# Kernel tuning notes

Hardware: AMD Instinct MI355X
Metric: run time of the kernel (lower is better)

## Reference

```python
import jax, jax.numpy as jnp
import numpy as np

N, K, GS = 11008, 4096, 128   # outfeatures, infeatures, group_size
INTER, KSTRIDE = 4, 64        # interleave, kstride from pack_intweight
B, S = 4, 2048
NG = K // GS                  # number of quantization groups


def _pack_np(q):
    """Replicates torch pack_intweight on an (N, K) int array of 4-bit values."""
    P = q.reshape(N, K // 32, 32)
    P = P.reshape(N, K // 32, 4, 4, 2).transpose(0, 1, 3, 2, 4).reshape(N, K // 32, 32)
    P = P.reshape(N, K // 32, 4, 8).reshape(N, K // 32, 4, 4, 2)
    P = P.transpose(0, 1, 2, 4, 3).reshape(N, K)
    P = P.reshape(N // INTER, INTER, K // KSTRIDE, KSTRIDE).transpose(0, 2, 1, 3)
    P = P.reshape(N // INTER, K // KSTRIDE, KSTRIDE, INTER)
    P = P[..., 0] | (P[..., 1] << 4) | (P[..., 2] << 8) | (P[..., 3] << 12)
    # uint16 bit pattern stored in int32 (schema has no int16)
    return P.reshape(N // INTER, K).astype(np.int32)


def setup_inputs() -> dict:
    rng = np.random.default_rng(0)
    q_unpacked = rng.integers(0, 16, size=(N, K), dtype=np.int64)  # int4 codes
    qweight = jnp.asarray(_pack_np(q_unpacked))

    key = jax.random.key(0)
    k1, k2, k3, k4 = jax.random.split(key, 4)
    x = jax.random.normal(k1, (B, S, K), dtype=jnp.float16)
    scales = (jax.random.uniform(k2, (NG, N), dtype=jnp.float32) * 0.01 + 0.005).astype(jnp.float16)
    scaled_zeros = (jax.random.normal(k3, (NG, N), dtype=jnp.float32) * 0.05).astype(jnp.float16)
    bias = (jax.random.normal(k4, (N,), dtype=jnp.float32) * 0.02).astype(jnp.float16)
    return {"x": x, "qweight": qweight, "scales": scales,
            "scaled_zeros": scaled_zeros, "bias": bias}


def _unpack(qweight):
    """Inverse of pack_intweight: (N//4, K) packed -> (N, K) int4 codes."""
    # split the 4 nibbles packed per 16-bit word
    nib = jnp.stack([(qweight >> (4 * i)) & 0xF for i in range(4)], axis=-1)  # (N//4, K, 4)
    # invert the interleave/kstride step
    t = nib.reshape(N // INTER, K // KSTRIDE, INTER, KSTRIDE)
    t = t.transpose(0, 2, 1, 3).reshape(N, K)
    # invert the second 32-lane shuffle
    t = t.reshape(N, K // 32, 4, 2, 4).transpose(0, 1, 2, 4, 3).reshape(N, K // 32, 32)
    # invert the first 32-lane shuffle
    t = t.reshape(N, K // 32, 4, 4, 2).transpose(0, 1, 3, 2, 4).reshape(N, K)
    return t


def reference(x, qweight, scales, scaled_zeros, bias):
    q = _unpack(qweight).astype(jnp.float16)                      # (N, K) codes 0..15
    s = scales.T[:, :, None]                                      # (N, NG, 1)
    z = scaled_zeros.T[:, :, None]                                # (N, NG, 1); stored as -zero*scale
    # w = q * scale + scaled_zeros  (== (q - zero) * scale)
    W = (q.reshape(N, NG, GS) * s + z).reshape(N, K)              # fp16 dequant
    return jnp.einsum('bsk,nk->bsn', x, W) + bias                 # (B, S, N)
```

## Files before the change

### kernel.cpp

```cpp
#include <hip/hip_runtime.h>
#include <hip/hip_bf16.h>

#define K_TOT 4096
#define N_TOT 11008
#define LDP 72

typedef __bf16 bf16x8 __attribute__((ext_vector_type(8)));
typedef float  f32x4  __attribute__((ext_vector_type(4)));
typedef float  f32x8  __attribute__((ext_vector_type(8)));

typedef __attribute__((address_space(1))) unsigned gu32;
typedef __attribute__((address_space(3))) unsigned lu32;

__device__ __forceinline__ void gload_lds16(const void* g, void* l) {
    __builtin_amdgcn_global_load_lds((gu32*)g, (lu32*)l, 16, 0, 0);
}

__global__ __launch_bounds__(256)
void dequant_w(const int* __restrict__ Qw, const float* __restrict__ Sc,
               const float* __restrict__ Zr, __bf16* __restrict__ Wb)
{
    const int t   = blockIdx.x * 256 + threadIdx.x;
    const int c8  = t & (K_TOT / 8 - 1);
    const int r4  = t >> 9;
    const int kp0 = c8 * 8;
    const int n   = r4 * 4 + ((kp0 >> 4) & 3);
    const int kq  = kp0 >> 6;
    const int hf  = (kp0 >> 3) & 1;
    const int kb  = kq * 64 + hf * 32;

    const int4 wa = *(const int4*)(Qw + (size_t)r4 * K_TOT + kp0);
    const int4 wb = *(const int4*)(Qw + (size_t)r4 * K_TOT + kp0 + 4);
    const int g = kb >> 7;
    const float s = Sc[(size_t)g * N_TOT + n];
    const float z = Zr[(size_t)g * N_TOT + n];

    const int w8[8] = {wa.x, wa.y, wa.z, wa.w, wb.x, wb.y, wb.z, wb.w};
    bf16x8 ov[4];
    #pragma unroll
    for (int uu = 0; uu < 8; ++uu) {
        const unsigned v = (unsigned)w8[uu] & 0xFFFFu;
        #pragma unroll
        for (int i = 0; i < 4; ++i)
            ov[i][uu] = (__bf16)fmaf((float)((v >> (4 * i)) & 0xFu), s, z);
    }
    __bf16* o = Wb + (size_t)n * K_TOT + kb;
    #pragma unroll
    for (int i = 0; i < 4; ++i) *(bf16x8*)(o + i * 8) = ov[i];
}

__global__ __launch_bounds__(256)
void convert_x(const float* __restrict__ X, __bf16* __restrict__ Xb, long total8)
{
    const long t = (long)blockIdx.x * 256 + threadIdx.x;
    if (t >= total8) return;
    f32x8 v = *(const f32x8*)(X + t * 8);
    bf16x8 o;
    #pragma unroll
    for (int j = 0; j < 8; ++j) o[j] = (__bf16)v[j];
    *(bf16x8*)(Xb + t * 8) = o;
}

__global__ __launch_bounds__(512, 2)
void gemm256(const __bf16* __restrict__ A, const __bf16* __restrict__ B,
             const float* __restrict__ Bias, float* __restrict__ C, int gridM)
{
    extern __shared__ char lds_raw[];

    const int tid  = threadIdx.x;
    const int lane = tid & 63;
    const int wid  = tid >> 6;
    const int l15  = lane & 15;
    const int lhi  = lane >> 4;

    const int nwg = gridDim.x;
    int wg = blockIdx.x;
    if ((nwg & 7) == 0) wg = (wg & 7) * (nwg >> 3) + (wg >> 3);
    const int bx  = wg % gridM;
    const int by  = wg / gridM;
    const int bm0 = bx * 256;
    const int bn0 = by * 256;

    const int wm = (wid >> 2) * 128;
    const int wn = (wid & 3) * 64;

    const int sr   = lane >> 3;
    const int scol = ((lane & 7) ^ sr) * 8;

    const __bf16* ap[4]; const __bf16* bp[4];
    #pragma unroll
    for (int j = 0; j < 4; ++j) {
        const int c = wid * 4 + j;
        ap[j] = A + (size_t)(bm0 + c * 8 + sr) * K_TOT + scol;
        bp[j] = B + (size_t)(bn0 + c * 8 + sr) * K_TOT + scol;
    }

    char* buf0 = lds_raw;
    char* buf1 = lds_raw + 65536;
    const int ldsoff = wid * 4096;

    const unsigned rswz = (unsigned)((l15 & 7) << 4);

    f32x4 acc[8][4] = {};

    #pragma unroll
    for (int j = 0; j < 4; ++j) {
        gload_lds16(ap[j], buf0 + ldsoff + j * 1024);
        gload_lds16(bp[j], buf0 + 32768 + ldsoff + j * 1024);
    }

    char* cur = buf0; char* nxt = buf1;
    const int NT = K_TOT / 64;
    for (int t = 0; t < NT; ++t) {
        if (t + 1 < NT) {
            const int k1 = (t + 1) * 64;
            #pragma unroll
            for (int j = 0; j < 4; ++j) {
                gload_lds16(ap[j] + k1, nxt + ldsoff + j * 1024);
                gload_lds16(bp[j] + k1, nxt + 32768 + ldsoff + j * 1024);
            }
            asm volatile("s_waitcnt vmcnt(8)" ::: "memory");
        } else {
            asm volatile("s_waitcnt vmcnt(0)" ::: "memory");
        }
        __builtin_amdgcn_s_barrier();
        __builtin_amdgcn_sched_barrier(0);

        #pragma unroll
        for (int ks = 0; ks < 2; ++ks) {
            bf16x8 af[8], bfv[4];
            const unsigned cb = ((unsigned)(ks * 64 + lhi * 16)) ^ rswz;
            #pragma unroll
            for (int mi = 0; mi < 8; ++mi)
                af[mi] = *(const bf16x8*)(cur + (wm + mi * 16 + l15) * 128 + cb);
            #pragma unroll
            for (int ni = 0; ni < 4; ++ni)
                bfv[ni] = *(const bf16x8*)(cur + 32768 + (wn + ni * 16 + l15) * 128 + cb);
            __builtin_amdgcn_s_setprio(1);
            #pragma unroll
            for (int mi = 0; mi < 8; ++mi)
                #pragma unroll
                for (int ni = 0; ni < 4; ++ni)
                    acc[mi][ni] = __builtin_amdgcn_mfma_f32_16x16x32_bf16(
                        af[mi], bfv[ni], acc[mi][ni], 0, 0, 0);
            __builtin_amdgcn_s_setprio(0);
        }
        asm volatile("" ::: "memory");
        __builtin_amdgcn_s_barrier();
        __builtin_amdgcn_sched_barrier(0);
        char* tmp = cur; cur = nxt; nxt = tmp;
    }

    #pragma unroll
    for (int ni = 0; ni < 4; ++ni) {
        const int col = bn0 + wn + ni * 16 + l15;
        const float bv = Bias[col];
        #pragma unroll
        for (int mi = 0; mi < 8; ++mi) {
            const int row = bm0 + wm + mi * 16 + lhi * 4;
            #pragma unroll
            for (int r = 0; r < 4; ++r)
                C[(size_t)(row + r) * N_TOT + col] = acc[mi][ni][r] + bv;
        }
    }
}

__global__ __launch_bounds__(256)
void qgemm_fused(const float* __restrict__ X, const int* __restrict__ Qw,
                 const float* __restrict__ Sc, const float* __restrict__ Zr,
                 const float* __restrict__ Bias, float* __restrict__ C)
{
    __shared__ __bf16 As[128][LDP];
    __shared__ __bf16 Bs[128][LDP];

    const int tid  = threadIdx.x;
    const int lane = tid & 63;
    const int wid  = tid >> 6;
    const int l15  = lane & 15;
    const int lhi  = lane >> 4;

    const int bm0 = blockIdx.x * 128;
    const int bn0 = blockIdx.y * 128;
    const int wm  = (wid >> 1) * 64;
    const int wn  = (wid & 1) * 64;

    const int ar = tid >> 3;
    const int ac = (tid & 7) * 8;

    const int nl   = tid >> 1;
    const int half = tid & 1;
    const int n_g  = bn0 + nl;
    const int* qptr = Qw + (size_t)(n_g >> 2) * K_TOT + (nl & 3) * 16 + half * 8;
    const float* scp = Sc + n_g;
    const float* zrp = Zr + n_g;

    f32x4 acc[4][4] = {};

    for (int kt = 0; kt < K_TOT / 64; ++kt) {
        const int k0 = kt * 64;
        const int4 wa = *(const int4*)(qptr + k0);
        const int4 wb = *(const int4*)(qptr + k0 + 4);
        const float s = scp[(size_t)(kt >> 1) * N_TOT];
        const float z = zrp[(size_t)(kt >> 1) * N_TOT];

        f32x8 av[4];
        #pragma unroll
        for (int p = 0; p < 4; ++p)
            av[p] = *(const f32x8*)(X + (size_t)(bm0 + p * 32 + ar) * K_TOT + k0 + ac);

        const int w8[8] = {wa.x, wa.y, wa.z, wa.w, wb.x, wb.y, wb.z, wb.w};
        bf16x8 ov[4];
        #pragma unroll
        for (int uu = 0; uu < 8; ++uu) {
            const unsigned v = (unsigned)w8[uu] & 0xFFFFu;
            #pragma unroll
            for (int i = 0; i < 4; ++i)
                ov[i][uu] = (__bf16)fmaf((float)((v >> (4 * i)) & 0xFu), s, z);
        }
        #pragma unroll
        for (int p = 0; p < 4; ++p) {
            bf16x8 ab;
            #pragma unroll
            for (int j = 0; j < 8; ++j) ab[j] = (__bf16)av[p][j];
            *(bf16x8*)&As[p * 32 + ar][ac] = ab;
        }
        #pragma unroll
        for (int cc = 0; cc < 4; ++cc)
            *(bf16x8*)&Bs[nl][half * 32 + cc * 8] = ov[cc];

        __syncthreads();

        #pragma unroll
        for (int ks = 0; ks < 2; ++ks) {
            bf16x8 af[4], bfr[4];
            const int kc = ks * 32 + lhi * 8;
            #pragma unroll
            for (int mi = 0; mi < 4; ++mi)
                af[mi] = *(const bf16x8*)&As[wm + mi * 16 + l15][kc];
            #pragma unroll
            for (int ni = 0; ni < 4; ++ni)
                bfr[ni] = *(const bf16x8*)&Bs[wn + ni * 16 + l15][kc];
            #pragma unroll
            for (int mi = 0; mi < 4; ++mi)
                #pragma unroll
                for (int ni = 0; ni < 4; ++ni)
                    acc[mi][ni] = __builtin_amdgcn_mfma_f32_16x16x32_bf16(
                        af[mi], bfr[ni], acc[mi][ni], 0, 0, 0);
        }
        __syncthreads();
    }

    #pragma unroll
    for (int ni = 0; ni < 4; ++ni) {
        const int col = bn0 + wn + ni * 16 + l15;
        const float bv = Bias[col];
        #pragma unroll
        for (int mi = 0; mi < 4; ++mi) {
            const int row = bm0 + wm + mi * 16 + lhi * 4;
            #pragma unroll
            for (int r = 0; r < 4; ++r)
                C[(size_t)(row + r) * N_TOT + col] = acc[mi][ni][r] + bv;
        }
    }
}

extern "C" void kernel_launch(void* const* d_in, const int* in_sizes, int n_in,
                              void* d_out, int out_size, void* d_ws, size_t ws_size,
                              hipStream_t stream) {
    const float* X    = (const float*)d_in[0];
    const int*   Qw   = (const int*)d_in[1];
    const float* Sc   = (const float*)d_in[2];
    const float* Zr   = (const float*)d_in[3];
    const float* Bias = (const float*)d_in[4];
    float* C = (float*)d_out;

    const int M = in_sizes[0] / K_TOT;
    const size_t xb_bytes = (size_t)M * K_TOT * 2;
    const size_t wb_bytes = (size_t)N_TOT * K_TOT * 2;
    const size_t need = xb_bytes + wb_bytes;

    const int gridM = M / 256;
    const int nwg   = gridM * (N_TOT / 256);

    if (ws_size >= need && (M & 255) == 0 && (nwg & 7) == 0) {
        __bf16* Xb = (__bf16*)d_ws;
        __bf16* Wb = (__bf16*)((char*)d_ws + xb_bytes);

        const int nW = (N_TOT / 4) * (K_TOT / 8);
        dequant_w<<<nW / 256, 256, 0, stream>>>(Qw, Sc, Zr, Wb);

        const long total8 = (long)M * K_TOT / 8;
        convert_x<<<(int)((total8 + 255) / 256), 256, 0, stream>>>(X, Xb, total8);

        (void)hipFuncSetAttribute((const void*)gemm256,
                                  hipFuncAttributeMaxDynamicSharedMemorySize, 131072);
        gemm256<<<dim3(nwg), dim3(512), 131072, stream>>>(Xb, Wb, Bias, C, gridM);
    } else {
        dim3 grid(M / 128, N_TOT / 128);
        qgemm_fused<<<grid, dim3(256), 0, stream>>>(X, Qw, Sc, Zr, Bias, C);
    }
}
```

Baseline: 925.8 us.

## Switch GEMM to 256x128 tiles with a three-stage LDS pipeline

```diff
diff --git a/kernel.cpp b/kernel.cpp
--- a/kernel.cpp
+++ b/kernel.cpp
@@ -61,9 +61,14 @@
     *(bf16x8*)(Xb + t * 8) = o;
 }
 
-__global__ __launch_bounds__(512, 2)
-void gemm256(const __bf16* __restrict__ A, const __bf16* __restrict__ B,
-             const float* __restrict__ Bias, float* __restrict__ C, int gridM)
+#define STAGE_A(kt, r, dst) \
+    gload_lds16(apg + (size_t)(r) * 64 * K_TOT + (size_t)(kt) * 64, (dst) + wid * 1024 + (r) * 8192)
+#define STAGE_B(kt, r, dst) \
+    gload_lds16(bpg + (size_t)(r) * 64 * K_TOT + (size_t)(kt) * 64, (dst) + 32768 + wid * 1024 + (r) * 8192)
+
+__global__ __launch_bounds__(512, 1)
+void gemm256x128(const __bf16* __restrict__ A, const __bf16* __restrict__ B,
+                 const float* __restrict__ Bias, float* __restrict__ C, int gridM)
 {
     extern __shared__ char lds_raw[];
 
@@ -75,80 +80,93 @@
 
     const int nwg = gridDim.x;
     int wg = blockIdx.x;
-    if ((nwg & 7) == 0) wg = (wg & 7) * (nwg >> 3) + (wg >> 3);
+    wg = (wg & 7) * (nwg >> 3) + (wg >> 3);
     const int bx  = wg % gridM;
     const int by  = wg / gridM;
     const int bm0 = bx * 256;
-    const int bn0 = by * 256;
-
-    const int wm = (wid >> 2) * 128;
-    const int wn = (wid & 3) * 64;
+    const int bn0 = by * 128;
+
+    const int wm = (wid >> 1) * 64;
+    const int wn = (wid & 1) * 64;
 
     const int sr   = lane >> 3;
     const int scol = ((lane & 7) ^ sr) * 8;
-
-    const __bf16* ap[4]; const __bf16* bp[4];
-    #pragma unroll
-    for (int j = 0; j < 4; ++j) {
-        const int c = wid * 4 + j;
-        ap[j] = A + (size_t)(bm0 + c * 8 + sr) * K_TOT + scol;
-        bp[j] = B + (size_t)(bn0 + c * 8 + sr) * K_TOT + scol;
-    }
-
-    char* buf0 = lds_raw;
-    char* buf1 = lds_raw + 65536;
-    const int ldsoff = wid * 4096;
+    const __bf16* apg = A + (size_t)(bm0 + wid * 8 + sr) * K_TOT + scol;
+    const __bf16* bpg = B + (size_t)(bn0 + wid * 8 + sr) * K_TOT + scol;
+
+    char* s0 = lds_raw;
+    char* s1 = lds_raw + 49152;
+    char* s2 = lds_raw + 98304;
 
     const unsigned rswz = (unsigned)((l15 & 7) << 4);
 
-    f32x4 acc[8][4] = {};
-
-    #pragma unroll
-    for (int j = 0; j < 4; ++j) {
-        gload_lds16(ap[j], buf0 + ldsoff + j * 1024);
-        gload_lds16(bp[j], buf0 + 32768 + ldsoff + j * 1024);
-    }
-
-    char* cur = buf0; char* nxt = buf1;
+    f32x4 acc[4][4] = {};
+
+    STAGE_A(0, 0, s0); STAGE_A(0, 1, s0); STAGE_A(0, 2, s0); STAGE_A(0, 3, s0);
+    STAGE_B(0, 0, s0); STAGE_B(0, 1, s0);
+    STAGE_A(1, 0, s1); STAGE_A(1, 1, s1); STAGE_A(1, 2, s1); STAGE_A(1, 3, s1);
+    STAGE_B(1, 0, s1); STAGE_B(1, 1, s1);
+    asm volatile("s_waitcnt vmcnt(6)" ::: "memory");
+    __builtin_amdgcn_s_barrier();
+
     const int NT = K_TOT / 64;
     for (int t = 0; t < NT; ++t) {
-        if (t + 1 < NT) {
-            const int k1 = (t + 1) * 64;
-            #pragma unroll
-            for (int j = 0; j < 4; ++j) {
-                gload_lds16(ap[j] + k1, nxt + ldsoff + j * 1024);
-                gload_lds16(bp[j] + k1, nxt + 32768 + ldsoff + j * 1024);
-            }
-            asm volatile("s_waitcnt vmcnt(8)" ::: "memory");
-        } else {
-            asm volatile("s_waitcnt vmcnt(0)" ::: "memory");
-        }
+        const int kt2 = (t + 2 < NT) ? t + 2 : NT - 1;
+
+        bf16x8 a8[4][2], bq0[2][2], bq1[2][2];
+
+        #pragma unroll
+        for (int kk = 0; kk < 2; ++kk) {
+            const unsigned cb = ((unsigned)(kk * 64 + lhi * 16)) ^ rswz;
+            #pragma unroll
+            for (int mi = 0; mi < 4; ++mi)
+                a8[mi][kk] = *(const bf16x8*)(s0 + (wm + mi * 16 + l15) * 128 + cb);
+            #pragma unroll
+            for (int nj = 0; nj < 2; ++nj)
+                bq0[nj][kk] = *(const bf16x8*)(s0 + 32768 + (wn + nj * 16 + l15) * 128 + cb);
+        }
+        STAGE_A(kt2, 0, s2); STAGE_A(kt2, 1, s2); STAGE_A(kt2, 2, s2);
+        asm volatile("s_waitcnt lgkmcnt(8)" ::: "memory");
         __builtin_amdgcn_s_barrier();
+        asm volatile("s_waitcnt lgkmcnt(0)" ::: "memory");
         __builtin_amdgcn_sched_barrier(0);
-
-        #pragma unroll
-        for (int ks = 0; ks < 2; ++ks) {
-            bf16x8 af[8], bfv[4];
-            const unsigned cb = ((unsigned)(ks * 64 + lhi * 16)) ^ rswz;
-            #pragma unroll
-            for (int mi = 0; mi < 8; ++mi)
-                af[mi] = *(const bf16x8*)(cur + (wm + mi * 16 + l15) * 128 + cb);
-            #pragma unroll
-            for (int ni = 0; ni < 4; ++ni)
-                bfv[ni] = *(const bf16x8*)(cur + 32768 + (wn + ni * 16 + l15) * 128 + cb);
-            __builtin_amdgcn_s_setprio(1);
-            #pragma unroll
-            for (int mi = 0; mi < 8; ++mi)
+        __builtin_amdgcn_s_setprio(1);
+        #pragma unroll
+        for (int mi = 0; mi < 4; ++mi)
+            #pragma unroll
+            for (int nj = 0; nj < 2; ++nj)
                 #pragma unroll
-                for (int ni = 0; ni < 4; ++ni)
-                    acc[mi][ni] = __builtin_amdgcn_mfma_f32_16x16x32_bf16(
-                        af[mi], bfv[ni], acc[mi][ni], 0, 0, 0);
-            __builtin_amdgcn_s_setprio(0);
-        }
-        asm volatile("" ::: "memory");
+                for (int kk = 0; kk < 2; ++kk)
+                    acc[mi][nj] = __builtin_amdgcn_mfma_f32_16x16x32_bf16(
+                        a8[mi][kk], bq0[nj][kk], acc[mi][nj], 0, 0, 0);
+        __builtin_amdgcn_s_setprio(0);
         __builtin_amdgcn_s_barrier();
+
+        #pragma unroll
+        for (int kk = 0; kk < 2; ++kk) {
+            const unsigned cb = ((unsigned)(kk * 64 + lhi * 16)) ^ rswz;
+            #pragma unroll
+            for (int nj = 0; nj < 2; ++nj)
+                bq1[nj][kk] = *(const bf16x8*)(s0 + 32768 + (wn + 32 + nj * 16 + l15) * 128 + cb);
+        }
+        STAGE_A(kt2, 3, s2); STAGE_B(kt2, 0, s2); STAGE_B(kt2, 1, s2);
+        asm volatile("s_waitcnt vmcnt(6)" ::: "memory");
+        __builtin_amdgcn_s_barrier();
+        asm volatile("s_waitcnt lgkmcnt(0)" ::: "memory");
         __builtin_amdgcn_sched_barrier(0);
-        char* tmp = cur; cur = nxt; nxt = tmp;
+        __builtin_amdgcn_s_setprio(1);
+        #pragma unroll
+        for (int mi = 0; mi < 4; ++mi)
+            #pragma unroll
+            for (int nj = 0; nj < 2; ++nj)
+                #pragma unroll
+                for (int kk = 0; kk < 2; ++kk)
+                    acc[mi][2 + nj] = __builtin_amdgcn_mfma_f32_16x16x32_bf16(
+                        a8[mi][kk], bq1[nj][kk], acc[mi][2 + nj], 0, 0, 0);
+        __builtin_amdgcn_s_setprio(0);
+        __builtin_amdgcn_s_barrier();
+
+        char* tmp = s0; s0 = s1; s1 = s2; s2 = tmp;
     }
 
     #pragma unroll
@@ -156,7 +174,7 @@
         const int col = bn0 + wn + ni * 16 + l15;
         const float bv = Bias[col];
         #pragma unroll
-        for (int mi = 0; mi < 8; ++mi) {
+        for (int mi = 0; mi < 4; ++mi) {
             const int row = bm0 + wm + mi * 16 + lhi * 4;
             #pragma unroll
             for (int r = 0; r < 4; ++r)
@@ -280,7 +298,7 @@
     const size_t need = xb_bytes + wb_bytes;
 
     const int gridM = M / 256;
-    const int nwg   = gridM * (N_TOT / 256);
+    const int nwg   = gridM * (N_TOT / 128);
 
     if (ws_size >= need && (M & 255) == 0 && (nwg & 7) == 0) {
         __bf16* Xb = (__bf16*)d_ws;
@@ -292,9 +310,9 @@
         const long total8 = (long)M * K_TOT / 8;
         convert_x<<<(int)((total8 + 255) / 256), 256, 0, stream>>>(X, Xb, total8);
 
-        (void)hipFuncSetAttribute((const void*)gemm256,
-                                  hipFuncAttributeMaxDynamicSharedMemorySize, 131072);
-        gemm256<<<dim3(nwg), dim3(512), 131072, stream>>>(Xb, Wb, Bias, C, gridM);
+        (void)hipFuncSetAttribute((const void*)gemm256x128,
+                                  hipFuncAttributeMaxDynamicSharedMemorySize, 147456);
+        gemm256x128<<<dim3(nwg), dim3(512), 147456, stream>>>(Xb, Wb, Bias, C, gridM);
     } else {
         dim3 grid(M / 128, N_TOT / 128);
         qgemm_fused<<<grid, dim3(256), 0, stream>>>(X, Qw, Sc, Zr, Bias, C);
```

Result: slower. 1.080 ms (+16.6%).

## Switch GEMM to K=32 tiles with 4-slot LDS ring and prefetch depth 2

Applied to the files above, without the earlier changes.

```diff
diff --git a/kernel.cpp b/kernel.cpp
--- a/kernel.cpp
+++ b/kernel.cpp
@@ -61,9 +61,17 @@
     *(bf16x8*)(Xb + t * 8) = o;
 }
 
-__global__ __launch_bounds__(512, 2)
-void gemm256(const __bf16* __restrict__ A, const __bf16* __restrict__ B,
-             const float* __restrict__ Bias, float* __restrict__ C, int gridM)
+#define STG(kt, sp) do {                                                    \
+    const size_t ko = (size_t)(kt) * 32;                                    \
+    gload_lds16(apg + ko,                        (sp) + wid * 2048);        \
+    gload_lds16(apg + ko + 16 * (size_t)K_TOT,   (sp) + wid * 2048 + 1024); \
+    gload_lds16(bpg + ko,                        (sp) + 16384 + wid * 2048);\
+    gload_lds16(bpg + ko + 16 * (size_t)K_TOT,   (sp) + 16384 + wid * 2048 + 1024); \
+} while (0)
+
+__global__ __launch_bounds__(512, 1)
+void gemm256k32(const __bf16* __restrict__ A, const __bf16* __restrict__ B,
+                const float* __restrict__ Bias, float* __restrict__ C, int gridM)
 {
     extern __shared__ char lds_raw[];
 
@@ -75,7 +83,7 @@
 
     const int nwg = gridDim.x;
     int wg = blockIdx.x;
-    if ((nwg & 7) == 0) wg = (wg & 7) * (nwg >> 3) + (wg >> 3);
+    wg = (wg & 7) * (nwg >> 3) + (wg >> 3);
     const int bx  = wg % gridM;
     const int by  = wg / gridM;
     const int bm0 = bx * 256;
@@ -84,71 +92,48 @@
     const int wm = (wid >> 2) * 128;
     const int wn = (wid & 3) * 64;
 
-    const int sr   = lane >> 3;
-    const int scol = ((lane & 7) ^ sr) * 8;
-
-    const __bf16* ap[4]; const __bf16* bp[4];
-    #pragma unroll
-    for (int j = 0; j < 4; ++j) {
-        const int c = wid * 4 + j;
-        ap[j] = A + (size_t)(bm0 + c * 8 + sr) * K_TOT + scol;
-        bp[j] = B + (size_t)(bn0 + c * 8 + sr) * K_TOT + scol;
-    }
-
-    char* buf0 = lds_raw;
-    char* buf1 = lds_raw + 65536;
-    const int ldsoff = wid * 4096;
-
-    const unsigned rswz = (unsigned)((l15 & 7) << 4);
+    const int srow = lane >> 2;
+    const int scol = (lane & 3) * 8;
+    const __bf16* apg = A + (size_t)(bm0 + wid * 32 + srow) * K_TOT + scol;
+    const __bf16* bpg = B + (size_t)(bn0 + wid * 32 + srow) * K_TOT + scol;
+
+    char* slot0 = lds_raw;
+    char* slot1 = lds_raw + 32768;
+    char* slot2 = lds_raw + 65536;
+    char* slot3 = lds_raw + 98304;
+    char* slots[4] = {slot0, slot1, slot2, slot3};
 
     f32x4 acc[8][4] = {};
 
-    #pragma unroll
-    for (int j = 0; j < 4; ++j) {
-        gload_lds16(ap[j], buf0 + ldsoff + j * 1024);
-        gload_lds16(bp[j], buf0 + 32768 + ldsoff + j * 1024);
-    }
-
-    char* cur = buf0; char* nxt = buf1;
-    const int NT = K_TOT / 64;
+    STG(0, slots[0]);
+    STG(1, slots[1]);
+
+    const int NT = K_TOT / 32;
     for (int t = 0; t < NT; ++t) {
-        if (t + 1 < NT) {
-            const int k1 = (t + 1) * 64;
-            #pragma unroll
-            for (int j = 0; j < 4; ++j) {
-                gload_lds16(ap[j] + k1, nxt + ldsoff + j * 1024);
-                gload_lds16(bp[j] + k1, nxt + 32768 + ldsoff + j * 1024);
-            }
-            asm volatile("s_waitcnt vmcnt(8)" ::: "memory");
-        } else {
-            asm volatile("s_waitcnt vmcnt(0)" ::: "memory");
-        }
+        const int t2 = (t + 2 < NT) ? t + 2 : NT - 1;
+        STG(t2, slots[(t + 2) & 3]);
+        asm volatile("s_waitcnt vmcnt(8)" ::: "memory");
         __builtin_amdgcn_s_barrier();
         __builtin_amdgcn_sched_barrier(0);
 
-        #pragma unroll
-        for (int ks = 0; ks < 2; ++ks) {
-            bf16x8 af[8], bfv[4];
-            const unsigned cb = ((unsigned)(ks * 64 + lhi * 16)) ^ rswz;
-            #pragma unroll
-            for (int mi = 0; mi < 8; ++mi)
-                af[mi] = *(const bf16x8*)(cur + (wm + mi * 16 + l15) * 128 + cb);
+        const char* s = slots[t & 3];
+        bf16x8 a8[8], b4[4];
+        #pragma unroll
+        for (int mi = 0; mi < 8; ++mi)
+            a8[mi] = *(const bf16x8*)(s + (wm + mi * 16 + l15) * 64 + lhi * 16);
+        #pragma unroll
+        for (int ni = 0; ni < 4; ++ni)
+            b4[ni] = *(const bf16x8*)(s + 16384 + (wn + ni * 16 + l15) * 64 + lhi * 16);
+        asm volatile("s_waitcnt lgkmcnt(0)" ::: "memory");
+        __builtin_amdgcn_sched_barrier(0);
+        __builtin_amdgcn_s_setprio(1);
+        #pragma unroll
+        for (int mi = 0; mi < 8; ++mi)
             #pragma unroll
             for (int ni = 0; ni < 4; ++ni)
-                bfv[ni] = *(const bf16x8*)(cur + 32768 + (wn + ni * 16 + l15) * 128 + cb);
-            __builtin_amdgcn_s_setprio(1);
-            #pragma unroll
-            for (int mi = 0; mi < 8; ++mi)
-                #pragma unroll
-                for (int ni = 0; ni < 4; ++ni)
-                    acc[mi][ni] = __builtin_amdgcn_mfma_f32_16x16x32_bf16(
-                        af[mi], bfv[ni], acc[mi][ni], 0, 0, 0);
-            __builtin_amdgcn_s_setprio(0);
-        }
-        asm volatile("" ::: "memory");
-        __builtin_amdgcn_s_barrier();
-        __builtin_amdgcn_sched_barrier(0);
-        char* tmp = cur; cur = nxt; nxt = tmp;
+                acc[mi][ni] = __builtin_amdgcn_mfma_f32_16x16x32_bf16(
+                    a8[mi], b4[ni], acc[mi][ni], 0, 0, 0);
+        __builtin_amdgcn_s_setprio(0);
     }
 
     #pragma unroll
@@ -292,9 +277,9 @@
         const long total8 = (long)M * K_TOT / 8;
         convert_x<<<(int)((total8 + 255) / 256), 256, 0, stream>>>(X, Xb, total8);
 
-        (void)hipFuncSetAttribute((const void*)gemm256,
+        (void)hipFuncSetAttribute((const void*)gemm256k32,
                                   hipFuncAttributeMaxDynamicSharedMemorySize, 131072);
-        gemm256<<<dim3(nwg), dim3(512), 131072, stream>>>(Xb, Wb, Bias, C, gridM);
+        gemm256k32<<<dim3(nwg), dim3(512), 131072, stream>>>(Xb, Wb, Bias, C, gridM);
     } else {
         dim3 grid(M / 128, N_TOT / 128);
         qgemm_fused<<<grid, dim3(256), 0, stream>>>(X, Qw, Sc, Zr, Bias, C);
```

New measurement: 1.203 ms. 29.9% more time.
